# Optimization experiments

Hardware: AMD Instinct MI355X
Metric: run time of the kernel (lower is better)

Reference implementation:

```python
import jax, jax.numpy as jnp
import numpy as np

N_NODES = 50000
N_EDGES = 800000
C = 256
R = 4

def setup_inputs() -> dict:
    key = jax.random.key(0)
    ks = jax.random.split(key, 8)
    node_features = jax.random.normal(ks[0], (N_NODES, C), dtype=jnp.float32)
    edge_index = jax.random.randint(ks[1], (2, N_EDGES), 0, N_NODES, dtype=jnp.int64)
    edge_type = jax.random.randint(ks[2], (N_EDGES,), 0, R, dtype=jnp.int64)
    # RGCNConv params (glorot-ish scale)
    s = 1.0 / np.sqrt(C)
    rel_weight = jax.random.normal(ks[3], (R, C, C), dtype=jnp.float32) * s
    root_weight = jax.random.normal(ks[4], (C, C), dtype=jnp.float32) * s
    rgcn_bias = jax.random.normal(ks[5], (C,), dtype=jnp.float32) * 0.01
    att_weight = jax.random.normal(ks[6], (1, 2 * C), dtype=jnp.float32) * (1.0 / np.sqrt(2 * C))
    att_bias = jax.random.normal(ks[7], (1,), dtype=jnp.float32) * 0.01
    return {
        'node_features': node_features,
        'edge_index': edge_index,
        'edge_type': edge_type,
        'rel_weight': rel_weight,
        'root_weight': root_weight,
        'rgcn_bias': rgcn_bias,
        'att_weight': att_weight,
        'att_bias': att_bias,
    }


def _rgcn(node_features, edge_index, edge_type, rel_weight, root_weight, rgcn_bias):
    # PyG RGCNConv: per-relation mean aggregation of x_src @ W_r, plus root transform + bias.
    N = node_features.shape[0]
    src, dst = edge_index[0], edge_index[1]
    out = node_features @ root_weight + rgcn_bias  # [N, O]
    num_rel = rel_weight.shape[0]
    for r in range(num_rel):  # small fixed relation count
        trans = node_features @ rel_weight[r]          # [N, O] node-level transform
        mask = (edge_type == r)
        msg = jnp.where(mask[:, None], trans[src], 0.0)  # [E, O] masked gather
        ssum = jax.ops.segment_sum(msg, dst, num_segments=N)
        cnt = jax.ops.segment_sum(mask.astype(node_features.dtype), dst, num_segments=N)
        out = out + ssum / jnp.maximum(cnt, 1.0)[:, None]  # mean aggr; 0 where no edges
    return out


def reference(node_features, edge_index, edge_type, rel_weight, root_weight, rgcn_bias, att_weight, att_bias):
    u0 = _rgcn(node_features, edge_index, edge_type, rel_weight, root_weight, rgcn_bias)
    cat = jnp.concatenate([u0, node_features], axis=1)  # [N, 2O]
    a = jax.nn.sigmoid(cat @ att_weight.T + att_bias)   # [N, 1]
    h = jnp.tanh(u0) * a + node_features * (1.0 - a)
    return h
```

## Files before the change

### kernel.cpp

```cpp
#include <hip/hip_runtime.h>
#include <hip/hip_bf16.h>

#define C 256
#define KTOT 1280
#define BM 64
#define BN 128
#define BK 32
#define NSTEP 40

typedef __attribute__((ext_vector_type(8))) short bf16x8;
typedef __attribute__((ext_vector_type(4))) float f32x4;
typedef __attribute__((ext_vector_type(4))) unsigned short us4;

#define GLL16(g, l)                                                         \
  __builtin_amdgcn_global_load_lds(                                         \
      (const __attribute__((address_space(1))) void*)(g),                   \
      (__attribute__((address_space(3))) void*)(l), 16, 0, 0)

__device__ __forceinline__ float bf2f(unsigned short u) {
  return __uint_as_float(((unsigned int)u) << 16);
}
__device__ __forceinline__ unsigned short f2bf(float f) {
  unsigned int x = __float_as_uint(f);
  unsigned int lsb = (x >> 16) & 1u;
  x += 0x7fffu + lsb;
  return (unsigned short)(x >> 16);
}

__global__ void k_pre(const float* __restrict__ X, const float* __restrict__ rel,
                      const float* __restrict__ root, unsigned short* __restrict__ Aall,
                      unsigned short* __restrict__ WT, int* __restrict__ cnt,
                      int N, int rowsPad) {
  int b = blockIdx.x, t = threadIdx.x;
  if (b < 1280) {
    int m = b >> 8, c = b & 255;
    const float* W = (m == 0) ? root : (rel + (size_t)(m - 1) * C * C);
    WT[(size_t)c * KTOT + m * C + t] = f2bf(W[(size_t)t * C + c]);
  } else if (b < 1280 + (rowsPad >> 2)) {
    int row = (b - 1280) * 4 + (t >> 6);
    int lane = t & 63;
    us4 o;
    if (row < N) {
      float4 v = reinterpret_cast<const float4*>(X + (size_t)row * C)[lane];
      o.x = f2bf(v.x); o.y = f2bf(v.y); o.z = f2bf(v.z); o.w = f2bf(v.w);
    } else { o.x = 0; o.y = 0; o.z = 0; o.w = 0; }
    *reinterpret_cast<us4*>(Aall + (size_t)row * KTOT + lane * 4) = o;
  } else {
    int i = (b - 1280 - (rowsPad >> 2)) * 256 + t;
    if (i < N) cnt[i] = 0;
  }
}

__global__ void k_hist(const int* __restrict__ edst, int* __restrict__ cnt, int E) {
  int e = blockIdx.x * blockDim.x + threadIdx.x;
  if (e < E) atomicAdd(cnt + edst[e], 1);
}

__global__ void k_scan1(const int* __restrict__ cnt, int* __restrict__ rp,
                        int* __restrict__ bsum, int n) {
  __shared__ int s[512];
  int t = threadIdx.x;
  int i = blockIdx.x * 512 + t;
  int v = (i < n) ? cnt[i] : 0;
  s[t] = v;
  __syncthreads();
  for (int off = 1; off < 512; off <<= 1) {
    int add = (t >= off) ? s[t - off] : 0;
    __syncthreads();
    s[t] += add;
    __syncthreads();
  }
  if (i < n) rp[i] = s[t] - v;
  if (t == 511) bsum[blockIdx.x] = s[511];
}

__global__ void k_scan2(const int* __restrict__ bsum, int* __restrict__ boff,
                        int* __restrict__ rp, int nb, int n) {
  if (threadIdx.x == 0) {
    int run = 0;
    for (int b = 0; b < nb; ++b) { boff[b] = run; run += bsum[b]; }
    rp[n] = run;
  }
}

__global__ void k_scan3(int* __restrict__ rp, const int* __restrict__ boff,
                        int* __restrict__ cursor, int n) {
  int i = blockIdx.x * 512 + threadIdx.x;
  if (i < n) {
    int v = rp[i] + boff[blockIdx.x];
    rp[i] = v;
    cursor[i] = v;
  }
}

__global__ void k_fill(const int* __restrict__ esrc, const int* __restrict__ edst,
                       const int* __restrict__ etype, int* __restrict__ cursor,
                       unsigned int* __restrict__ sorted, int E) {
  int e = blockIdx.x * blockDim.x + threadIdx.x;
  if (e >= E) return;
  int d = edst[e];
  int pos = atomicAdd(cursor + d, 1);
  sorted[pos] = (unsigned int)esrc[e] | ((unsigned int)etype[e] << 28);
}

#define ACC(u, v)                                                            \
  do {                                                                       \
    float f0 = bf2f((v).x), f1 = bf2f((v).y), f2 = bf2f((v).z), f3 = bf2f((v).w); \
    switch ((u) >> 28) {                                                     \
      case 0: a0.x += f0; a0.y += f1; a0.z += f2; a0.w += f3; ++c0; break;   \
      case 1: a1.x += f0; a1.y += f1; a1.z += f2; a1.w += f3; ++c1; break;   \
      case 2: a2.x += f0; a2.y += f1; a2.z += f2; a2.w += f3; ++c2; break;   \
      default: a3.x += f0; a3.y += f1; a3.z += f2; a3.w += f3; ++c3; break;  \
    }                                                                        \
  } while (0)

__global__ void k_gather(unsigned short* __restrict__ Aall,
                         const unsigned int* __restrict__ sorted,
                         const int* __restrict__ rp, int N, int rowsPad) {
  int wave = threadIdx.x >> 6;
  int lane = threadIdx.x & 63;
  int dst = blockIdx.x * 4 + wave;
  if (dst >= rowsPad) return;
  us4* agv = reinterpret_cast<us4*>(Aall);

  if (dst >= N) {
    us4 z; z.x = 0; z.y = 0; z.z = 0; z.w = 0;
    for (int r = 1; r <= 4; ++r)
      agv[(size_t)dst * 320 + r * 64 + lane] = z;
    return;
  }

  float4 a0 = make_float4(0, 0, 0, 0), a1 = a0, a2 = a0, a3 = a0;
  int c0 = 0, c1 = 0, c2 = 0, c3 = 0;
  int s = rp[dst], e2 = rp[dst + 1];

  int e = s;
  for (; e + 8 <= e2; e += 8) {
    unsigned int u0 = sorted[e],     u1 = sorted[e + 1], u2 = sorted[e + 2], u3 = sorted[e + 3];
    unsigned int u4 = sorted[e + 4], u5 = sorted[e + 5], u6 = sorted[e + 6], u7 = sorted[e + 7];
    us4 v0 = agv[(size_t)(u0 & 0x0FFFFFFFu) * 320 + lane];
    us4 v1 = agv[(size_t)(u1 & 0x0FFFFFFFu) * 320 + lane];
    us4 v2 = agv[(size_t)(u2 & 0x0FFFFFFFu) * 320 + lane];
    us4 v3 = agv[(size_t)(u3 & 0x0FFFFFFFu) * 320 + lane];
    us4 v4 = agv[(size_t)(u4 & 0x0FFFFFFFu) * 320 + lane];
    us4 v5 = agv[(size_t)(u5 & 0x0FFFFFFFu) * 320 + lane];
    us4 v6 = agv[(size_t)(u6 & 0x0FFFFFFFu) * 320 + lane];
    us4 v7 = agv[(size_t)(u7 & 0x0FFFFFFFu) * 320 + lane];
    ACC(u0, v0); ACC(u1, v1); ACC(u2, v2); ACC(u3, v3);
    ACC(u4, v4); ACC(u5, v5); ACC(u6, v6); ACC(u7, v7);
  }
  for (; e + 4 <= e2; e += 4) {
    unsigned int u0 = sorted[e], u1 = sorted[e + 1], u2 = sorted[e + 2], u3 = sorted[e + 3];
    us4 v0 = agv[(size_t)(u0 & 0x0FFFFFFFu) * 320 + lane];
    us4 v1 = agv[(size_t)(u1 & 0x0FFFFFFFu) * 320 + lane];
    us4 v2 = agv[(size_t)(u2 & 0x0FFFFFFFu) * 320 + lane];
    us4 v3 = agv[(size_t)(u3 & 0x0FFFFFFFu) * 320 + lane];
    ACC(u0, v0); ACC(u1, v1); ACC(u2, v2); ACC(u3, v3);
  }
  for (; e < e2; ++e) {
    unsigned int u = sorted[e];
    us4 v = agv[(size_t)(u & 0x0FFFFFFFu) * 320 + lane];
    ACC(u, v);
  }

  float s0 = 1.0f / (float)max(c0, 1);
  float s1 = 1.0f / (float)max(c1, 1);
  float s2 = 1.0f / (float)max(c2, 1);
  float s3 = 1.0f / (float)max(c3, 1);
  us4 o;
  size_t base = (size_t)dst * 320 + lane;
  o.x = f2bf(a0.x * s0); o.y = f2bf(a0.y * s0); o.z = f2bf(a0.z * s0); o.w = f2bf(a0.w * s0);
  agv[base + 64] = o;
  o.x = f2bf(a1.x * s1); o.y = f2bf(a1.y * s1); o.z = f2bf(a1.z * s1); o.w = f2bf(a1.w * s1);
  agv[base + 128] = o;
  o.x = f2bf(a2.x * s2); o.y = f2bf(a2.y * s2); o.z = f2bf(a2.z * s2); o.w = f2bf(a2.w * s2);
  agv[base + 192] = o;
  o.x = f2bf(a3.x * s3); o.y = f2bf(a3.y * s3); o.z = f2bf(a3.z * s3); o.w = f2bf(a3.w * s3);
  agv[base + 256] = o;
}

__global__ __launch_bounds__(256) void k_gemm(
    const unsigned short* __restrict__ Aall, const unsigned short* __restrict__ WT,
    const float* __restrict__ bias, float* __restrict__ out, int N, int rowsPad) {
  __shared__ unsigned short lds_a[2][BM * BK];
  __shared__ unsigned short lds_b[2][BN * BK];
  int tid = threadIdx.x;
  int wave = tid >> 6, lane = tid & 63;

  int nwg = gridDim.x, orig = blockIdx.x;
  int q = nwg >> 3, r = nwg & 7;
  int xcd = orig & 7, lin = orig >> 3;
  int wgid = (xcd < r ? xcd * (q + 1) : r * (q + 1) + (xcd - r) * q) + lin;
  int mblk = wgid >> 1, nblk = wgid & 1;
  int row0 = mblk * BM, col0 = nblk * BN;
  int wr = wave >> 1, wc = wave & 1, lcol = lane & 15;

  int offA = wave * 1024 + lane * 16;
  int arS = offA >> 6;
  int alg8 = ((((offA >> 4) & 3) ^ ((arS >> 1) & 3))) * 8;
  const unsigned short* aSrc = Aall + (size_t)(row0 + arS) * KTOT + alg8;
  const unsigned short* bSrc[2];
#pragma unroll
  for (int c2 = 0; c2 < 2; ++c2) {
    int off = (wave * 2 + c2) * 1024 + lane * 16;
    int rr = off >> 6;
    int lg8 = ((((off >> 4) & 3) ^ ((rr >> 1) & 3))) * 8;
    bSrc[c2] = WT + (size_t)(col0 + rr) * KTOT + lg8;
  }

  int aoff[2], boff[4];
  int kb = (lane >> 4) * 16;
#pragma unroll
  for (int i = 0; i < 2; ++i) {
    int ar = wr * 32 + i * 16 + lcol;
    aoff[i] = ar * 64 + (kb ^ (((ar >> 1) & 3) << 4));
  }
#pragma unroll
  for (int j = 0; j < 4; ++j) {
    int bc = wc * 64 + j * 16 + lcol;
    boff[j] = bc * 64 + (kb ^ (((bc >> 1) & 3) << 4));
  }

  f32x4 acc[2][4];
#pragma unroll
  for (int i = 0; i < 2; ++i)
#pragma unroll
    for (int j = 0; j < 4; ++j) {
      f32x4 z; z[0] = 0.f; z[1] = 0.f; z[2] = 0.f; z[3] = 0.f;
      acc[i][j] = z;
    }

  auto stage = [&](int buf, int ks) {
    int kofs = ks * BK;
    GLL16(aSrc + kofs, (char*)&lds_a[buf][0] + wave * 1024);
    GLL16(bSrc[0] + kofs, (char*)&lds_b[buf][0] + (wave * 2) * 1024);
    GLL16(bSrc[1] + kofs, (char*)&lds_b[buf][0] + (wave * 2 + 1) * 1024);
  };

  stage(0, 0);
  __syncthreads();

#pragma unroll 1
  for (int ks = 0; ks < NSTEP; ++ks) {
    int cur = ks & 1;
    if (ks + 1 < NSTEP) stage(cur ^ 1, ks + 1);
    bf16x8 af[2], bfr[4];
#pragma unroll
    for (int i = 0; i < 2; ++i)
      af[i] = *reinterpret_cast<const bf16x8*>((const char*)&lds_a[cur][0] + aoff[i]);
#pragma unroll
    for (int j = 0; j < 4; ++j)
      bfr[j] = *reinterpret_cast<const bf16x8*>((const char*)&lds_b[cur][0] + boff[j]);
#pragma unroll
    for (int mr = 0; mr < 2; ++mr)
#pragma unroll
      for (int nc = 0; nc < 4; ++nc)
        acc[mr][nc] = __builtin_amdgcn_mfma_f32_16x16x32_bf16(af[mr], bfr[nc], acc[mr][nc], 0, 0, 0);
    __syncthreads();
  }

  int lrow4 = (lane >> 4) * 4;
#pragma unroll
  for (int mr = 0; mr < 2; ++mr) {
#pragma unroll
    for (int reg = 0; reg < 4; ++reg) {
      int rowg = row0 + wr * 32 + mr * 16 + lrow4 + reg;
      if (rowg < N) {
#pragma unroll
        for (int nc = 0; nc < 4; ++nc) {
          int colg = col0 + wc * 64 + nc * 16 + lcol;
          out[(size_t)rowg * C + colg] = acc[mr][nc][reg] + bias[colg];
        }
      }
    }
  }
}

__global__ void k_gate(const float* __restrict__ X, const float* __restrict__ aw,
                       const float* __restrict__ ab, float* __restrict__ out, int N) {
  int wave = threadIdx.x >> 6, lane = threadIdx.x & 63;
  int node = blockIdx.x * 4 + wave;
  if (node >= N) return;
  const float4* u4 = reinterpret_cast<const float4*>(out + (size_t)node * C);
  const float4* x4 = reinterpret_cast<const float4*>(X + (size_t)node * C);
  float4 u = u4[lane], x = x4[lane];
  const float4* w = reinterpret_cast<const float4*>(aw);
  float4 w1 = w[lane], w2 = w[64 + lane];
  float p = u.x * w1.x + u.y * w1.y + u.z * w1.z + u.w * w1.w
          + x.x * w2.x + x.y * w2.y + x.z * w2.z + x.w * w2.w;
#pragma unroll
  for (int off = 32; off >= 1; off >>= 1) p += __shfl_xor(p, off);
  float a = 1.0f / (1.0f + expf(-(p + ab[0])));
  float b = 1.0f - a;
  float4 h;
  h.x = tanhf(u.x) * a + x.x * b;
  h.y = tanhf(u.y) * a + x.y * b;
  h.z = tanhf(u.z) * a + x.z * b;
  h.w = tanhf(u.w) * a + x.w * b;
  reinterpret_cast<float4*>(out + (size_t)node * C)[lane] = h;
}

extern "C" void kernel_launch(void* const* d_in, const int* in_sizes, int n_in,
                              void* d_out, int out_size, void* d_ws, size_t ws_size,
                              hipStream_t stream) {
  const float* X     = (const float*)d_in[0];
  const int*   eidx  = (const int*)d_in[1];
  const int*   etype = (const int*)d_in[2];
  const float* rel   = (const float*)d_in[3];
  const float* root  = (const float*)d_in[4];
  const float* bias  = (const float*)d_in[5];
  const float* attw  = (const float*)d_in[6];
  const float* ab    = (const float*)d_in[7];
  float* out = (float*)d_out;

  int N = in_sizes[0] / C;
  int E = in_sizes[2];
  int rowsPad = ((N + 127) / 128) * 128;
  const int* esrc = eidx;
  const int* edst = eidx + E;

  char* w = (char*)d_ws;
  size_t off = 0;
  auto alloc = [&](size_t bytes) -> void* {
    void* p = w + off;
    off += (bytes + 255) & ~(size_t)255;
    return p;
  };
  unsigned short* Aall = (unsigned short*)alloc((size_t)rowsPad * KTOT * 2);
  unsigned short* WT   = (unsigned short*)alloc((size_t)C * KTOT * 2);
  int* cnt    = (int*)alloc((size_t)N * 4);
  int* rp     = (int*)alloc((size_t)(N + 1) * 4);
  int* cursor = (int*)alloc((size_t)N * 4);
  int* bsum   = (int*)alloc(1024);
  int* boffb  = (int*)alloc(1024);
  unsigned int* sorted = (unsigned int*)alloc((size_t)E * 4);

  int preBlocks = 1280 + (rowsPad >> 2) + (N + 255) / 256;
  k_pre<<<preBlocks, 256, 0, stream>>>(X, rel, root, Aall, WT, cnt, N, rowsPad);
  k_hist<<<(E + 255) / 256, 256, 0, stream>>>(edst, cnt, E);
  int NB = (N + 511) / 512;
  k_scan1<<<NB, 512, 0, stream>>>(cnt, rp, bsum, N);
  k_scan2<<<1, 64, 0, stream>>>(bsum, boffb, rp, NB, N);
  k_scan3<<<NB, 512, 0, stream>>>(rp, boffb, cursor, N);
  k_fill<<<(E + 255) / 256, 256, 0, stream>>>(esrc, edst, etype, cursor, sorted, E);
  k_gather<<<rowsPad / 4, 256, 0, stream>>>(Aall, sorted, rp, N, rowsPad);
  k_gemm<<<(rowsPad / BM) * 2, 256, 0, stream>>>(Aall, WT, bias, out, N, rowsPad);
  k_gate<<<(N + 3) / 4, 256, 0, stream>>>(X, attw, ab, out, N);
}
```

Baseline: 272.2 us.

## Transform nodes before aggregation and fuse gather with root, bias and gate

The order changes from aggregate-then-GEMM (K=1280) to GEMM-then-aggregate. All five weight matrices are applied to X first, giving a bf16 Y of shape N×1280. The gather kernel then reads the relation slice of Y for each edge and fuses the mean, root term, bias, attention gate and tanh, which removes the separate gate kernel and the fp32 intermediate round trip. The X half of the attention dot product is computed during preprocessing. In exchange, the gather reads from a wider Y array, and rounding the transformed features to bf16 before averaging changes the numerics.

```diff
diff --git a/kernel.cpp b/kernel.cpp
--- a/kernel.cpp
+++ b/kernel.cpp
@@ -2,11 +2,8 @@
 #include <hip/hip_bf16.h>
 
 #define C 256
-#define KTOT 1280
-#define BM 64
-#define BN 128
+#define NOUT 1280
 #define BK 32
-#define NSTEP 40
 
 typedef __attribute__((ext_vector_type(8))) short bf16x8;
 typedef __attribute__((ext_vector_type(4))) float f32x4;
@@ -28,25 +25,35 @@
 }
 
 __global__ void k_pre(const float* __restrict__ X, const float* __restrict__ rel,
-                      const float* __restrict__ root, unsigned short* __restrict__ Aall,
-                      unsigned short* __restrict__ WT, int* __restrict__ cnt,
+                      const float* __restrict__ root, const float* __restrict__ attw,
+                      unsigned short* __restrict__ Xbf, unsigned short* __restrict__ WT2,
+                      float* __restrict__ ax2, int* __restrict__ cnt,
                       int N, int rowsPad) {
   int b = blockIdx.x, t = threadIdx.x;
-  if (b < 1280) {
+  if (b < NOUT) {
     int m = b >> 8, c = b & 255;
     const float* W = (m == 0) ? root : (rel + (size_t)(m - 1) * C * C);
-    WT[(size_t)c * KTOT + m * C + t] = f2bf(W[(size_t)t * C + c]);
-  } else if (b < 1280 + (rowsPad >> 2)) {
-    int row = (b - 1280) * 4 + (t >> 6);
+    WT2[(size_t)b * C + t] = f2bf(W[(size_t)t * C + c]);
+  } else if (b < NOUT + (rowsPad >> 2)) {
+    int row = (b - NOUT) * 4 + (t >> 6);
     int lane = t & 63;
-    us4 o;
     if (row < N) {
       float4 v = reinterpret_cast<const float4*>(X + (size_t)row * C)[lane];
+      float4 w2 = reinterpret_cast<const float4*>(attw + C)[lane];
+      us4 o;
       o.x = f2bf(v.x); o.y = f2bf(v.y); o.z = f2bf(v.z); o.w = f2bf(v.w);
-    } else { o.x = 0; o.y = 0; o.z = 0; o.w = 0; }
-    *reinterpret_cast<us4*>(Aall + (size_t)row * KTOT + lane * 4) = o;
+      reinterpret_cast<us4*>(Xbf)[(size_t)row * 64 + lane] = o;
+      float p = v.x * w2.x + v.y * w2.y + v.z * w2.z + v.w * w2.w;
+#pragma unroll
+      for (int m2 = 32; m2 >= 1; m2 >>= 1) p += __shfl_xor(p, m2);
+      if (lane == 0) ax2[row] = p;
+    } else if (row < rowsPad) {
+      us4 z; z.x = 0; z.y = 0; z.z = 0; z.w = 0;
+      reinterpret_cast<us4*>(Xbf)[(size_t)row * 64 + lane] = z;
+      if (lane == 0) ax2[row] = 0.f;
+    }
   } else {
-    int i = (b - 1280 - (rowsPad >> 2)) * 256 + t;
+    int i = (b - NOUT - (rowsPad >> 2)) * 256 + t;
     if (i < N) cnt[i] = 0;
   }
 }
@@ -103,6 +110,99 @@
   sorted[pos] = (unsigned int)esrc[e] | ((unsigned int)etype[e] << 28);
 }
 
+__global__ __launch_bounds__(256) void k_gemm(
+    const unsigned short* __restrict__ Xbf, const unsigned short* __restrict__ WT2,
+    unsigned short* __restrict__ Y, int rowsPad) {
+  __shared__ unsigned short lds_a[2][128 * BK];
+  __shared__ unsigned short lds_b[2][128 * BK];
+  int tid = threadIdx.x;
+  int wave = tid >> 6, lane = tid & 63;
+
+  int nwg = gridDim.x, orig = blockIdx.x;
+  int q = nwg >> 3, r = nwg & 7;
+  int xcd = orig & 7, lin = orig >> 3;
+  int wgid = (xcd < r ? xcd * (q + 1) : r * (q + 1) + (xcd - r) * q) + lin;
+  int mblk = wgid / 10, nblk = wgid - mblk * 10;
+  int row0 = mblk * 128, col0 = nblk * 128;
+  int wr = wave >> 1, wc = wave & 1, lcol = lane & 15;
+
+  const unsigned short* aSrc[2];
+  const unsigned short* bSrc[2];
+  int ldsOfs[2];
+#pragma unroll
+  for (int c2 = 0; c2 < 2; ++c2) {
+    int off = (wave * 2 + c2) * 1024 + lane * 16;
+    int rr = off >> 6;
+    int lg8 = (((off >> 4) & 3) ^ ((rr >> 1) & 3)) * 8;
+    aSrc[c2] = Xbf + (size_t)(row0 + rr) * C + lg8;
+    bSrc[c2] = WT2 + (size_t)(col0 + rr) * C + lg8;
+    ldsOfs[c2] = (wave * 2 + c2) * 1024;
+  }
+
+  int aoff[4], boff[4];
+  int kb = (lane >> 4) * 16;
+#pragma unroll
+  for (int i = 0; i < 4; ++i) {
+    int ar = wr * 64 + i * 16 + lcol;
+    aoff[i] = ar * 64 + (kb ^ (((ar >> 1) & 3) << 4));
+    int bc = wc * 64 + i * 16 + lcol;
+    boff[i] = bc * 64 + (kb ^ (((bc >> 1) & 3) << 4));
+  }
+
+  f32x4 acc[4][4];
+#pragma unroll
+  for (int i = 0; i < 4; ++i)
+#pragma unroll
+    for (int j = 0; j < 4; ++j) {
+      f32x4 z; z[0] = 0.f; z[1] = 0.f; z[2] = 0.f; z[3] = 0.f;
+      acc[i][j] = z;
+    }
+
+  auto stage = [&](int buf, int ks) {
+    int kofs = ks * BK;
+#pragma unroll
+    for (int c2 = 0; c2 < 2; ++c2) {
+      GLL16(aSrc[c2] + kofs, (char*)&lds_a[buf][0] + ldsOfs[c2]);
+      GLL16(bSrc[c2] + kofs, (char*)&lds_b[buf][0] + ldsOfs[c2]);
+    }
+  };
+
+  stage(0, 0);
+  __syncthreads();
+
+#pragma unroll 2
+  for (int ks = 0; ks < 8; ++ks) {
+    int cur = ks & 1;
+    if (ks + 1 < 8) stage(cur ^ 1, ks + 1);
+    bf16x8 af[4], bfr[4];
+#pragma unroll
+    for (int i = 0; i < 4; ++i) {
+      af[i]  = *reinterpret_cast<const bf16x8*>((const char*)&lds_a[cur][0] + aoff[i]);
+      bfr[i] = *reinterpret_cast<const bf16x8*>((const char*)&lds_b[cur][0] + boff[i]);
+    }
+#pragma unroll
+    for (int mr = 0; mr < 4; ++mr)
+#pragma unroll
+      for (int nc = 0; nc < 4; ++nc)
+        acc[mr][nc] = __builtin_amdgcn_mfma_f32_16x16x32_bf16(af[mr], bfr[nc], acc[mr][nc], 0, 0, 0);
+    __syncthreads();
+  }
+
+  int lrow4 = (lane >> 4) * 4;
+#pragma unroll
+  for (int mr = 0; mr < 4; ++mr) {
+#pragma unroll
+    for (int reg = 0; reg < 4; ++reg) {
+      int rowg = row0 + wr * 64 + mr * 16 + lrow4 + reg;
+#pragma unroll
+      for (int nc = 0; nc < 4; ++nc) {
+        int colg = col0 + wc * 64 + nc * 16 + lcol;
+        Y[(size_t)rowg * NOUT + colg] = f2bf(acc[mr][nc][reg]);
+      }
+    }
+  }
+}
+
 #define ACC(u, v)                                                            \
   do {                                                                       \
     float f0 = bf2f((v).x), f1 = bf2f((v).y), f2 = bf2f((v).z), f3 = bf2f((v).w); \
@@ -114,190 +214,68 @@
     }                                                                        \
   } while (0)
 
-__global__ void k_gather(unsigned short* __restrict__ Aall,
-                         const unsigned int* __restrict__ sorted,
-                         const int* __restrict__ rp, int N, int rowsPad) {
-  int wave = threadIdx.x >> 6;
-  int lane = threadIdx.x & 63;
+__global__ void k_gg(const unsigned short* __restrict__ Y,
+                     const unsigned int* __restrict__ sorted,
+                     const int* __restrict__ rp, const float* __restrict__ X,
+                     const float* __restrict__ bias, const float* __restrict__ attw,
+                     const float* __restrict__ abp, const float* __restrict__ ax2,
+                     float* __restrict__ out, int N) {
+  int wave = threadIdx.x >> 6, lane = threadIdx.x & 63;
   int dst = blockIdx.x * 4 + wave;
-  if (dst >= rowsPad) return;
-  us4* agv = reinterpret_cast<us4*>(Aall);
-
-  if (dst >= N) {
-    us4 z; z.x = 0; z.y = 0; z.z = 0; z.w = 0;
-    for (int r = 1; r <= 4; ++r)
-      agv[(size_t)dst * 320 + r * 64 + lane] = z;
-    return;
-  }
+  if (dst >= N) return;
+  const us4* Yv = reinterpret_cast<const us4*>(Y);
 
   float4 a0 = make_float4(0, 0, 0, 0), a1 = a0, a2 = a0, a3 = a0;
   int c0 = 0, c1 = 0, c2 = 0, c3 = 0;
   int s = rp[dst], e2 = rp[dst + 1];
 
+#define YIDX(u) ((size_t)((u) & 0x0FFFFFFFu) * 320 + (((u) >> 28) + 1) * 64 + lane)
   int e = s;
   for (; e + 8 <= e2; e += 8) {
     unsigned int u0 = sorted[e],     u1 = sorted[e + 1], u2 = sorted[e + 2], u3 = sorted[e + 3];
     unsigned int u4 = sorted[e + 4], u5 = sorted[e + 5], u6 = sorted[e + 6], u7 = sorted[e + 7];
-    us4 v0 = agv[(size_t)(u0 & 0x0FFFFFFFu) * 320 + lane];
-    us4 v1 = agv[(size_t)(u1 & 0x0FFFFFFFu) * 320 + lane];
-    us4 v2 = agv[(size_t)(u2 & 0x0FFFFFFFu) * 320 + lane];
-    us4 v3 = agv[(size_t)(u3 & 0x0FFFFFFFu) * 320 + lane];
-    us4 v4 = agv[(size_t)(u4 & 0x0FFFFFFFu) * 320 + lane];
-    us4 v5 = agv[(size_t)(u5 & 0x0FFFFFFFu) * 320 + lane];
-    us4 v6 = agv[(size_t)(u6 & 0x0FFFFFFFu) * 320 + lane];
-    us4 v7 = agv[(size_t)(u7 & 0x0FFFFFFFu) * 320 + lane];
+    us4 v0 = Yv[YIDX(u0)], v1 = Yv[YIDX(u1)], v2 = Yv[YIDX(u2)], v3 = Yv[YIDX(u3)];
+    us4 v4 = Yv[YIDX(u4)], v5 = Yv[YIDX(u5)], v6 = Yv[YIDX(u6)], v7 = Yv[YIDX(u7)];
     ACC(u0, v0); ACC(u1, v1); ACC(u2, v2); ACC(u3, v3);
     ACC(u4, v4); ACC(u5, v5); ACC(u6, v6); ACC(u7, v7);
   }
   for (; e + 4 <= e2; e += 4) {
     unsigned int u0 = sorted[e], u1 = sorted[e + 1], u2 = sorted[e + 2], u3 = sorted[e + 3];
-    us4 v0 = agv[(size_t)(u0 & 0x0FFFFFFFu) * 320 + lane];
-    us4 v1 = agv[(size_t)(u1 & 0x0FFFFFFFu) * 320 + lane];
-    us4 v2 = agv[(size_t)(u2 & 0x0FFFFFFFu) * 320 + lane];
-    us4 v3 = agv[(size_t)(u3 & 0x0FFFFFFFu) * 320 + lane];
+    us4 v0 = Yv[YIDX(u0)], v1 = Yv[YIDX(u1)], v2 = Yv[YIDX(u2)], v3 = Yv[YIDX(u3)];
     ACC(u0, v0); ACC(u1, v1); ACC(u2, v2); ACC(u3, v3);
   }
   for (; e < e2; ++e) {
     unsigned int u = sorted[e];
-    us4 v = agv[(size_t)(u & 0x0FFFFFFFu) * 320 + lane];
+    us4 v = Yv[YIDX(u)];
     ACC(u, v);
   }
+#undef YIDX
 
   float s0 = 1.0f / (float)max(c0, 1);
   float s1 = 1.0f / (float)max(c1, 1);
   float s2 = 1.0f / (float)max(c2, 1);
   float s3 = 1.0f / (float)max(c3, 1);
-  us4 o;
-  size_t base = (size_t)dst * 320 + lane;
-  o.x = f2bf(a0.x * s0); o.y = f2bf(a0.y * s0); o.z = f2bf(a0.z * s0); o.w = f2bf(a0.w * s0);
-  agv[base + 64] = o;
-  o.x = f2bf(a1.x * s1); o.y = f2bf(a1.y * s1); o.z = f2bf(a1.z * s1); o.w = f2bf(a1.w * s1);
-  agv[base + 128] = o;
-  o.x = f2bf(a2.x * s2); o.y = f2bf(a2.y * s2); o.z = f2bf(a2.z * s2); o.w = f2bf(a2.w * s2);
-  agv[base + 192] = o;
-  o.x = f2bf(a3.x * s3); o.y = f2bf(a3.y * s3); o.z = f2bf(a3.z * s3); o.w = f2bf(a3.w * s3);
-  agv[base + 256] = o;
-}
-
-__global__ __launch_bounds__(256) void k_gemm(
-    const unsigned short* __restrict__ Aall, const unsigned short* __restrict__ WT,
-    const float* __restrict__ bias, float* __restrict__ out, int N, int rowsPad) {
-  __shared__ unsigned short lds_a[2][BM * BK];
-  __shared__ unsigned short lds_b[2][BN * BK];
-  int tid = threadIdx.x;
-  int wave = tid >> 6, lane = tid & 63;
-
-  int nwg = gridDim.x, orig = blockIdx.x;
-  int q = nwg >> 3, r = nwg & 7;
-  int xcd = orig & 7, lin = orig >> 3;
-  int wgid = (xcd < r ? xcd * (q + 1) : r * (q + 1) + (xcd - r) * q) + lin;
-  int mblk = wgid >> 1, nblk = wgid & 1;
-  int row0 = mblk * BM, col0 = nblk * BN;
-  int wr = wave >> 1, wc = wave & 1, lcol = lane & 15;
-
-  int offA = wave * 1024 + lane * 16;
-  int arS = offA >> 6;
-  int alg8 = ((((offA >> 4) & 3) ^ ((arS >> 1) & 3))) * 8;
-  const unsigned short* aSrc = Aall + (size_t)(row0 + arS) * KTOT + alg8;
-  const unsigned short* bSrc[2];
-#pragma unroll
-  for (int c2 = 0; c2 < 2; ++c2) {
-    int off = (wave * 2 + c2) * 1024 + lane * 16;
-    int rr = off >> 6;
-    int lg8 = ((((off >> 4) & 3) ^ ((rr >> 1) & 3))) * 8;
-    bSrc[c2] = WT + (size_t)(col0 + rr) * KTOT + lg8;
-  }
-
-  int aoff[2], boff[4];
-  int kb = (lane >> 4) * 16;
-#pragma unroll
-  for (int i = 0; i < 2; ++i) {
-    int ar = wr * 32 + i * 16 + lcol;
-    aoff[i] = ar * 64 + (kb ^ (((ar >> 1) & 3) << 4));
-  }
-#pragma unroll
-  for (int j = 0; j < 4; ++j) {
-    int bc = wc * 64 + j * 16 + lcol;
-    boff[j] = bc * 64 + (kb ^ (((bc >> 1) & 3) << 4));
-  }
-
-  f32x4 acc[2][4];
-#pragma unroll
-  for (int i = 0; i < 2; ++i)
-#pragma unroll
-    for (int j = 0; j < 4; ++j) {
-      f32x4 z; z[0] = 0.f; z[1] = 0.f; z[2] = 0.f; z[3] = 0.f;
-      acc[i][j] = z;
-    }
-
-  auto stage = [&](int buf, int ks) {
-    int kofs = ks * BK;
-    GLL16(aSrc + kofs, (char*)&lds_a[buf][0] + wave * 1024);
-    GLL16(bSrc[0] + kofs, (char*)&lds_b[buf][0] + (wave * 2) * 1024);
-    GLL16(bSrc[1] + kofs, (char*)&lds_b[buf][0] + (wave * 2 + 1) * 1024);
-  };
-
-  stage(0, 0);
-  __syncthreads();
-
-#pragma unroll 1
-  for (int ks = 0; ks < NSTEP; ++ks) {
-    int cur = ks & 1;
-    if (ks + 1 < NSTEP) stage(cur ^ 1, ks + 1);
-    bf16x8 af[2], bfr[4];
-#pragma unroll
-    for (int i = 0; i < 2; ++i)
-      af[i] = *reinterpret_cast<const bf16x8*>((const char*)&lds_a[cur][0] + aoff[i]);
-#pragma unroll
-    for (int j = 0; j < 4; ++j)
-      bfr[j] = *reinterpret_cast<const bf16x8*>((const char*)&lds_b[cur][0] + boff[j]);
-#pragma unroll
-    for (int mr = 0; mr < 2; ++mr)
-#pragma unroll
-      for (int nc = 0; nc < 4; ++nc)
-        acc[mr][nc] = __builtin_amdgcn_mfma_f32_16x16x32_bf16(af[mr], bfr[nc], acc[mr][nc], 0, 0, 0);
-    __syncthreads();
-  }
-
-  int lrow4 = (lane >> 4) * 4;
-#pragma unroll
-  for (int mr = 0; mr < 2; ++mr) {
-#pragma unroll
-    for (int reg = 0; reg < 4; ++reg) {
-      int rowg = row0 + wr * 32 + mr * 16 + lrow4 + reg;
-      if (rowg < N) {
-#pragma unroll
-        for (int nc = 0; nc < 4; ++nc) {
-          int colg = col0 + wc * 64 + nc * 16 + lcol;
-          out[(size_t)rowg * C + colg] = acc[mr][nc][reg] + bias[colg];
-        }
-      }
-    }
-  }
-}
-
-__global__ void k_gate(const float* __restrict__ X, const float* __restrict__ aw,
-                       const float* __restrict__ ab, float* __restrict__ out, int N) {
-  int wave = threadIdx.x >> 6, lane = threadIdx.x & 63;
-  int node = blockIdx.x * 4 + wave;
-  if (node >= N) return;
-  const float4* u4 = reinterpret_cast<const float4*>(out + (size_t)node * C);
-  const float4* x4 = reinterpret_cast<const float4*>(X + (size_t)node * C);
-  float4 u = u4[lane], x = x4[lane];
-  const float4* w = reinterpret_cast<const float4*>(aw);
-  float4 w1 = w[lane], w2 = w[64 + lane];
-  float p = u.x * w1.x + u.y * w1.y + u.z * w1.z + u.w * w1.w
-          + x.x * w2.x + x.y * w2.y + x.z * w2.z + x.w * w2.w;
-#pragma unroll
-  for (int off = 32; off >= 1; off >>= 1) p += __shfl_xor(p, off);
-  float a = 1.0f / (1.0f + expf(-(p + ab[0])));
+  us4 rt = Yv[(size_t)dst * 320 + lane];
+  float4 bi = reinterpret_cast<const float4*>(bias)[lane];
+  float4 w1 = reinterpret_cast<const float4*>(attw)[lane];
+  float4 u0;
+  u0.x = a0.x * s0 + a1.x * s1 + a2.x * s2 + a3.x * s3 + bf2f(rt.x) + bi.x;
+  u0.y = a0.y * s0 + a1.y * s1 + a2.y * s2 + a3.y * s3 + bf2f(rt.y) + bi.y;
+  u0.z = a0.z * s0 + a1.z * s1 + a2.z * s2 + a3.z * s3 + bf2f(rt.z) + bi.z;
+  u0.w = a0.w * s0 + a1.w * s1 + a2.w * s2 + a3.w * s3 + bf2f(rt.w) + bi.w;
+
+  float p = u0.x * w1.x + u0.y * w1.y + u0.z * w1.z + u0.w * w1.w;
+#pragma unroll
+  for (int m2 = 32; m2 >= 1; m2 >>= 1) p += __shfl_xor(p, m2);
+  float a = 1.0f / (1.0f + expf(-(p + ax2[dst] + abp[0])));
   float b = 1.0f - a;
+  float4 x4 = reinterpret_cast<const float4*>(X + (size_t)dst * C)[lane];
   float4 h;
-  h.x = tanhf(u.x) * a + x.x * b;
-  h.y = tanhf(u.y) * a + x.y * b;
-  h.z = tanhf(u.z) * a + x.z * b;
-  h.w = tanhf(u.w) * a + x.w * b;
-  reinterpret_cast<float4*>(out + (size_t)node * C)[lane] = h;
+  h.x = tanhf(u0.x) * a + x4.x * b;
+  h.y = tanhf(u0.y) * a + x4.y * b;
+  h.z = tanhf(u0.z) * a + x4.z * b;
+  h.w = tanhf(u0.w) * a + x4.w * b;
+  reinterpret_cast<float4*>(out + (size_t)dst * C)[lane] = h;
 }
 
 extern "C" void kernel_launch(void* const* d_in, const int* in_sizes, int n_in,
@@ -326,8 +304,10 @@
     off += (bytes + 255) & ~(size_t)255;
     return p;
   };
-  unsigned short* Aall = (unsigned short*)alloc((size_t)rowsPad * KTOT * 2);
-  unsigned short* WT   = (unsigned short*)alloc((size_t)C * KTOT * 2);
+  unsigned short* Y    = (unsigned short*)alloc((size_t)rowsPad * NOUT * 2);
+  unsigned short* Xbf  = (unsigned short*)alloc((size_t)rowsPad * C * 2);
+  unsigned short* WT2  = (unsigned short*)alloc((size_t)NOUT * C * 2);
+  float* ax2  = (float*)alloc((size_t)rowsPad * 4);
   int* cnt    = (int*)alloc((size_t)N * 4);
   int* rp     = (int*)alloc((size_t)(N + 1) * 4);
   int* cursor = (int*)alloc((size_t)N * 4);
@@ -335,15 +315,14 @@
   int* boffb  = (int*)alloc(1024);
   unsigned int* sorted = (unsigned int*)alloc((size_t)E * 4);
 
-  int preBlocks = 1280 + (rowsPad >> 2) + (N + 255) / 256;
-  k_pre<<<preBlocks, 256, 0, stream>>>(X, rel, root, Aall, WT, cnt, N, rowsPad);
+  int preBlocks = NOUT + (rowsPad >> 2) + (N + 255) / 256;
+  k_pre<<<preBlocks, 256, 0, stream>>>(X, rel, root, attw, Xbf, WT2, ax2, cnt, N, rowsPad);
+  k_gemm<<<(rowsPad / 128) * 10, 256, 0, stream>>>(Xbf, WT2, Y, rowsPad);
   k_hist<<<(E + 255) / 256, 256, 0, stream>>>(edst, cnt, E);
   int NB = (N + 511) / 512;
   k_scan1<<<NB, 512, 0, stream>>>(cnt, rp, bsum, N);
   k_scan2<<<1, 64, 0, stream>>>(bsum, boffb, rp, NB, N);
   k_scan3<<<NB, 512, 0, stream>>>(rp, boffb, cursor, N);
   k_fill<<<(E + 255) / 256, 256, 0, stream>>>(esrc, edst, etype, cursor, sorted, E);
-  k_gather<<<rowsPad / 4, 256, 0, stream>>>(Aall, sorted, rp, N, rowsPad);
-  k_gemm<<<(rowsPad / BM) * 2, 256, 0, stream>>>(Aall, WT, bias, out, N, rowsPad);
-  k_gate<<<(N + 3) / 4, 256, 0, stream>>>(X, attw, ab, out, N);
-}
+  k_gg<<<(N + 3) / 4, 256, 0, stream>>>(Y, sorted, rp, X, bias, attw, ab, ax2, out, N);
+}
```

New measurement: 256.9 us. -5.6%, faster.
